# Performance work log

Hardware: AMD Instinct MI355X
Metric: run time of the kernel (lower is better)

The kernel has to match this reference:

```python
import jax, jax.numpy as jnp
import numpy as np

EPS = 1e-8
ALPHA = 0.3
PATTERN_W = 0.1


def setup_inputs() -> dict:
    key = jax.random.key(0)
    ks = jax.random.split(key, 6)
    H, W, D, Hid = 1024, 1024, 32, 64
    return {
        "grid_states": jax.random.normal(ks[0], (H, W, D), dtype=jnp.float32),
        "potentials": jax.random.uniform(ks[1], (H, W), dtype=jnp.float32),
        "W1": jax.random.normal(ks[2], (D + 1, Hid), dtype=jnp.float32) * 0.1,
        "b1": jax.random.normal(ks[3], (Hid,), dtype=jnp.float32) * 0.1,
        "W2": jax.random.normal(ks[4], (Hid, D), dtype=jnp.float32) * 0.1,
        "b2": jax.random.normal(ks[5], (D,), dtype=jnp.float32) * 0.1,
    }


def reference(grid_states, potentials, W1, b1, W2, b2):
    # self_similarity: A^3 normalized to unit length, rescaled by ||A||
    cube = grid_states * grid_states * grid_states                     # [H,W,D]
    cube_norm = jnp.linalg.norm(cube, axis=-1, keepdims=True)          # [H,W,1]
    cell_norm = jnp.linalg.norm(grid_states, axis=-1, keepdims=True)   # [H,W,1]
    self_pattern = cube / (cube_norm + EPS) * cell_norm                # [H,W,D]

    cell_with_pattern = grid_states + PATTERN_W * self_pattern         # [H,W,D]

    # transform_net on [cell_with_pattern ; potential]
    x = jnp.concatenate([cell_with_pattern, potentials[..., None]], axis=-1)  # [H,W,D+1]
    h = jax.nn.relu(jnp.einsum("hwc,cf->hwf", x, W1) + b1)             # [H,W,Hid]
    transformed = jnp.einsum("hwf,fd->hwd", h, W2) + b2                # [H,W,D]

    # new_state = transform + alpha * cell  (neighbor influence path only
    # affects role_value, which forward() discards)
    return transformed + ALPHA * grid_states
```

## Files before the change

### kernel.cpp

```cpp
#include <hip/hip_runtime.h>

#define DIM   32
#define HID   64
#define TILES 8
#define HPAD  72
#define HBUF  (16 * HPAD)

typedef __attribute__((ext_vector_type(8))) short bf16x8;
typedef __attribute__((ext_vector_type(4))) float f32x4;

__device__ __forceinline__ unsigned cvt_pk_bf16(float lo, float hi) {
    unsigned r;
    asm("v_cvt_pk_bf16_f32 %0, %1, %2" : "=v"(r) : "v"(lo), "v"(hi));
    return r;
}

union bfu { bf16x8 v; unsigned u[4]; };

__global__ __launch_bounds__(256) void behavior_mfma(
    const float* __restrict__ g_in,
    const float* __restrict__ pot,
    const float* __restrict__ W1,
    const float* __restrict__ b1,
    const float* __restrict__ W2,
    const float* __restrict__ b2,
    float* __restrict__ out)
{
    __shared__ __align__(16) short sH[4 * 2 * HBUF];

    const int tid  = threadIdx.x;
    const int lane = tid & 63;
    const int quad = lane >> 4;
    const int mrow = lane & 15;
    const int wave = tid >> 6;
    short* hb = &sH[wave * 2 * HBUF];

    bf16x8 w1f[4];
    float  w1p[4], b1v[4];
    #pragma unroll
    for (int nb = 0; nb < 4; ++nb) {
        bfu t;
        #pragma unroll
        for (int jp = 0; jp < 4; ++jp)
            t.u[jp] = cvt_pk_bf16(W1[(quad * 8 + 2 * jp)     * HID + nb * 16 + mrow],
                                  W1[(quad * 8 + 2 * jp + 1) * HID + nb * 16 + mrow]);
        w1f[nb] = t.v;
        w1p[nb] = W1[32 * HID + nb * 16 + mrow];
        b1v[nb] = b1[nb * 16 + mrow];
    }
    bf16x8 w2f[2][2];
    #pragma unroll
    for (int kc = 0; kc < 2; ++kc)
        #pragma unroll
        for (int nc = 0; nc < 2; ++nc) {
            bfu t;
            #pragma unroll
            for (int jp = 0; jp < 4; ++jp)
                t.u[jp] = cvt_pk_bf16(W2[(kc * 32 + quad * 8 + 2 * jp)     * DIM + nc * 16 + mrow],
                                      W2[(kc * 32 + quad * 8 + 2 * jp + 1) * DIM + nc * 16 + mrow]);
            w2f[kc][nc] = t.v;
        }
    float b2v[2];
    #pragma unroll
    for (int nc = 0; nc < 2; ++nc) b2v[nc] = b2[nc * 16 + mrow];

    bf16x8 idf[2];
    #pragma unroll
    for (int nc = 0; nc < 2; ++nc) {
        bfu t;
        #pragma unroll
        for (int jp = 0; jp < 4; ++jp) {
            unsigned lo = (quad * 8 + 2 * jp     == nc * 16 + mrow) ? 0x00003F80u : 0u;
            unsigned hi = (quad * 8 + 2 * jp + 1 == nc * 16 + mrow) ? 0x3F800000u : 0u;
            t.u[jp] = lo | hi;
        }
        idf[nc] = t.v;
    }

    const long cell0 = ((long)blockIdx.x * 4 + wave) * (TILES * 16);

    auto loadTile = [&](long cb, float4& a, float4& b, float4& p) {
        const float* gp = g_in + (cb + mrow) * DIM + quad * 8;
        a = ((const float4*)gp)[0];
        b = ((const float4*)gp)[1];
        p = *(const float4*)(pot + cb + quad * 4);
    };

    auto stageA = [&](const float4& a, const float4& b, const float4& p,
                      short* buf, bf16x8& gf_out) {
        float gv[8] = {a.x, a.y, a.z, a.w, b.x, b.y, b.z, b.w};
        float cube[8];
        float tp = 0.f, sp = 0.f;
        #pragma unroll
        for (int j = 0; j < 8; ++j) {
            float gc = gv[j];
            float g2 = gc * gc;
            float g3 = g2 * gc;
            tp += g2;
            sp = fmaf(g3, g3, sp);
            cube[j] = g3;
        }
        tp += __shfl_xor(tp, 16, 64); tp += __shfl_xor(tp, 32, 64);
        sp += __shfl_xor(sp, 16, 64); sp += __shfl_xor(sp, 32, 64);
        const float scale = 0.1f * __builtin_amdgcn_sqrtf(tp) *
                            __builtin_amdgcn_rcpf(__builtin_amdgcn_sqrtf(sp) + 1e-8f);

        bfu xf, gf;
        #pragma unroll
        for (int jp = 0; jp < 4; ++jp) {
            xf.u[jp] = cvt_pk_bf16(fmaf(scale, cube[2 * jp],     gv[2 * jp]),
                                   fmaf(scale, cube[2 * jp + 1], gv[2 * jp + 1]));
            gf.u[jp] = cvt_pk_bf16(0.3f * gv[2 * jp], 0.3f * gv[2 * jp + 1]);
        }
        gf_out = gf.v;

        const float pvr[4] = {p.x, p.y, p.z, p.w};
        #pragma unroll
        for (int nb = 0; nb < 4; ++nb) {
            f32x4 c1;
            #pragma unroll
            for (int r = 0; r < 4; ++r) c1[r] = fmaf(pvr[r], w1p[nb], b1v[nb]);
            c1 = __builtin_amdgcn_mfma_f32_16x16x32_bf16(xf.v, w1f[nb], c1, 0, 0, 0);
            unsigned p01 = cvt_pk_bf16(fmaxf(c1[0], 0.f), fmaxf(c1[1], 0.f));
            unsigned p23 = cvt_pk_bf16(fmaxf(c1[2], 0.f), fmaxf(c1[3], 0.f));
            short* bp = &buf[(quad * 4) * HPAD + nb * 16 + mrow];
            bp[0 * HPAD] = (short)(p01);
            bp[1 * HPAD] = (short)(p01 >> 16);
            bp[2 * HPAD] = (short)(p23);
            bp[3 * HPAD] = (short)(p23 >> 16);
        }
    };

    auto gemm2 = [&](const bf16x8& hf0, const bf16x8& hf1, const bf16x8& gfv, long cb) {
        #pragma unroll
        for (int nc = 0; nc < 2; ++nc) {
            f32x4 c2 = {b2v[nc], b2v[nc], b2v[nc], b2v[nc]};
            c2 = __builtin_amdgcn_mfma_f32_16x16x32_bf16(gfv, idf[nc],    c2, 0, 0, 0);
            c2 = __builtin_amdgcn_mfma_f32_16x16x32_bf16(hf0, w2f[0][nc], c2, 0, 0, 0);
            c2 = __builtin_amdgcn_mfma_f32_16x16x32_bf16(hf1, w2f[1][nc], c2, 0, 0, 0);
            #pragma unroll
            for (int r = 0; r < 4; ++r)
                out[(cb + quad * 4 + r) * DIM + nc * 16 + mrow] = c2[r];
        }
    };

    float4 cga, cgb, cpv, nga, ngb, npv;
    bf16x8 gfP, gfC;

    loadTile(cell0, cga, cgb, cpv);
    loadTile(cell0 + 16, nga, ngb, npv);
    stageA(cga, cgb, cpv, hb, gfP);

    #pragma unroll 2
    for (int t = 1; t < TILES; ++t) {
        short* rbuf = hb + ((t - 1) & 1) * HBUF;
        bf16x8 hf0 = *(const bf16x8*)&rbuf[mrow * HPAD +  0 + quad * 8];
        bf16x8 hf1 = *(const bf16x8*)&rbuf[mrow * HPAD + 32 + quad * 8];

        cga = nga; cgb = ngb; cpv = npv;
        if (t + 1 < TILES)
            loadTile(cell0 + (long)(t + 1) * 16, nga, ngb, npv);

        stageA(cga, cgb, cpv, hb + (t & 1) * HBUF, gfC);

        gemm2(hf0, hf1, gfP, cell0 + (long)(t - 1) * 16);
        gfP = gfC;
    }

    {
        short* rbuf = hb + ((TILES - 1) & 1) * HBUF;
        bf16x8 hf0 = *(const bf16x8*)&rbuf[mrow * HPAD +  0 + quad * 8];
        bf16x8 hf1 = *(const bf16x8*)&rbuf[mrow * HPAD + 32 + quad * 8];
        gemm2(hf0, hf1, gfP, cell0 + (long)(TILES - 1) * 16);
    }
}

extern "C" void kernel_launch(void* const* d_in, const int* in_sizes, int n_in,
                              void* d_out, int out_size, void* d_ws, size_t ws_size,
                              hipStream_t stream) {
    const float* g_in = (const float*)d_in[0];
    const float* pot  = (const float*)d_in[1];
    const float* W1   = (const float*)d_in[2];
    const float* b1   = (const float*)d_in[3];
    const float* W2   = (const float*)d_in[4];
    const float* b2   = (const float*)d_in[5];
    float* out = (float*)d_out;

    const int n_cells = in_sizes[1];
    const int cells_per_block = 4 * TILES * 16;
    const int blocks = (n_cells + cells_per_block - 1) / cells_per_block;

    behavior_mfma<<<blocks, 256, 0, stream>>>(g_in, pot, W1, b1, W2, b2, out);
}
```

Before: 247.2 us.

## Compute transposed MFMA products and pass hidden activations via permlane swaps instead of LDS

Swaps the MFMA operand order so each lane holds results for its own cell row, then rebuilds the second GEMM's hidden-activation fragments in registers with permlane32 swaps and a permuted W2 row order, removing the LDS buffer and its scalar stores and vector reloads. The row-sum reductions use a permlane swap in place of one cross-lane shuffle. Output is written as 16-byte nontemporal vector stores per lane instead of scattered scalar stores, and launch bounds request 4 blocks per CU. Removing LDS staging also drops the software pipelining across tiles, so MFMA and memory latency overlap now depends on occupancy.

Measured after the change: 256.2 us. 1.04x slower.

```diff
diff --git a/kernel.cpp b/kernel.cpp
--- a/kernel.cpp
+++ b/kernel.cpp
@@ -3,8 +3,6 @@
 #define DIM   32
 #define HID   64
 #define TILES 8
-#define HPAD  72
-#define HBUF  (16 * HPAD)
 
 typedef __attribute__((ext_vector_type(8))) short bf16x8;
 typedef __attribute__((ext_vector_type(4))) float f32x4;
@@ -15,9 +13,22 @@
     return r;
 }
 
+__device__ __forceinline__ void plswap(unsigned &a, unsigned &b) {
+    auto r = __builtin_amdgcn_permlane32_swap((int)a, (int)b, false, false);
+    a = (unsigned)r[0];
+    b = (unsigned)r[1];
+}
+
+__device__ __forceinline__ float quad_sum(float x) {
+    unsigned a = __float_as_uint(x), b = __float_as_uint(x);
+    plswap(a, b);
+    float t = __uint_as_float(a) + __uint_as_float(b);
+    return t + __shfl_xor(t, 16, 64);
+}
+
 union bfu { bf16x8 v; unsigned u[4]; };
 
-__global__ __launch_bounds__(256) void behavior_mfma(
+__global__ __launch_bounds__(256, 4) void behavior_mfma(
     const float* __restrict__ g_in,
     const float* __restrict__ pot,
     const float* __restrict__ W1,
@@ -26,17 +37,13 @@
     const float* __restrict__ b2,
     float* __restrict__ out)
 {
-    __shared__ __align__(16) short sH[4 * 2 * HBUF];
-
     const int tid  = threadIdx.x;
     const int lane = tid & 63;
     const int quad = lane >> 4;
     const int mrow = lane & 15;
     const int wave = tid >> 6;
-    short* hb = &sH[wave * 2 * HBUF];
 
     bf16x8 w1f[4];
-    float  w1p[4], b1v[4];
     #pragma unroll
     for (int nb = 0; nb < 4; ++nb) {
         bfu t;
@@ -45,8 +52,6 @@
             t.u[jp] = cvt_pk_bf16(W1[(quad * 8 + 2 * jp)     * HID + nb * 16 + mrow],
                                   W1[(quad * 8 + 2 * jp + 1) * HID + nb * 16 + mrow]);
         w1f[nb] = t.v;
-        w1p[nb] = W1[32 * HID + nb * 16 + mrow];
-        b1v[nb] = b1[nb * 16 + mrow];
     }
     bf16x8 w2f[2][2];
     #pragma unroll
@@ -55,16 +60,16 @@
         for (int nc = 0; nc < 2; ++nc) {
             bfu t;
             #pragma unroll
-            for (int jp = 0; jp < 4; ++jp)
-                t.u[jp] = cvt_pk_bf16(W2[(kc * 32 + quad * 8 + 2 * jp)     * DIM + nc * 16 + mrow],
-                                      W2[(kc * 32 + quad * 8 + 2 * jp + 1) * DIM + nc * 16 + mrow]);
+            for (int jp = 0; jp < 4; ++jp) {
+                const int j0 = 2 * jp;
+                const int r0 = kc * 32 + (quad >> 1) * 16 + (quad & 1) * 4
+                             + ((j0 >> 2) << 3) + (j0 & 3);
+                t.u[jp] = cvt_pk_bf16(W2[r0 * DIM + nc * 16 + mrow],
+                                      W2[(r0 + 1) * DIM + nc * 16 + mrow]);
+            }
             w2f[kc][nc] = t.v;
         }
-    float b2v[2];
-    #pragma unroll
-    for (int nc = 0; nc < 2; ++nc) b2v[nc] = b2[nc * 16 + mrow];
-
-    bf16x8 idf[2];
+    bf16x8 aid[2];
     #pragma unroll
     for (int nc = 0; nc < 2; ++nc) {
         bfu t;
@@ -74,20 +79,42 @@
             unsigned hi = (quad * 8 + 2 * jp + 1 == nc * 16 + mrow) ? 0x3F800000u : 0u;
             t.u[jp] = lo | hi;
         }
-        idf[nc] = t.v;
+        aid[nc] = t.v;
     }
+    float w1pq[4][4], b1q[4][4];
+    #pragma unroll
+    for (int nb = 0; nb < 4; ++nb)
+        #pragma unroll
+        for (int r = 0; r < 4; ++r) {
+            w1pq[nb][r] = W1[32 * HID + nb * 16 + quad * 4 + r];
+            b1q[nb][r]  = b1[nb * 16 + quad * 4 + r];
+        }
+    float b2q[2][4];
+    #pragma unroll
+    for (int nc = 0; nc < 2; ++nc)
+        #pragma unroll
+        for (int r = 0; r < 4; ++r)
+            b2q[nc][r] = b2[nc * 16 + quad * 4 + r];
 
     const long cell0 = ((long)blockIdx.x * 4 + wave) * (TILES * 16);
 
-    auto loadTile = [&](long cb, float4& a, float4& b, float4& p) {
+    float4 gA[2], gB[2]; float pV[2];
+    auto loadT = [&](long cb, int s) {
         const float* gp = g_in + (cb + mrow) * DIM + quad * 8;
-        a = ((const float4*)gp)[0];
-        b = ((const float4*)gp)[1];
-        p = *(const float4*)(pot + cb + quad * 4);
+        gA[s] = ((const float4*)gp)[0];
+        gB[s] = ((const float4*)gp)[1];
+        pV[s] = pot[cb + mrow];
     };
+    loadT(cell0, 0);
+    loadT(cell0 + 16, 1);
 
-    auto stageA = [&](const float4& a, const float4& b, const float4& p,
-                      short* buf, bf16x8& gf_out) {
+    #pragma unroll 2
+    for (int t = 0; t < TILES; ++t) {
+        const int s = t & 1;
+        const long cb = cell0 + (long)t * 16;
+        const float4 a = gA[s], b = gB[s];
+        const float potv = pV[s];
+
         float gv[8] = {a.x, a.y, a.z, a.w, b.x, b.y, b.z, b.w};
         float cube[8];
         float tp = 0.f, sp = 0.f;
@@ -100,8 +127,8 @@
             sp = fmaf(g3, g3, sp);
             cube[j] = g3;
         }
-        tp += __shfl_xor(tp, 16, 64); tp += __shfl_xor(tp, 32, 64);
-        sp += __shfl_xor(sp, 16, 64); sp += __shfl_xor(sp, 32, 64);
+        tp = quad_sum(tp);
+        sp = quad_sum(sp);
         const float scale = 0.1f * __builtin_amdgcn_sqrtf(tp) *
                             __builtin_amdgcn_rcpf(__builtin_amdgcn_sqrtf(sp) + 1e-8f);
 
@@ -112,66 +139,42 @@
                                    fmaf(scale, cube[2 * jp + 1], gv[2 * jp + 1]));
             gf.u[jp] = cvt_pk_bf16(0.3f * gv[2 * jp], 0.3f * gv[2 * jp + 1]);
         }
-        gf_out = gf.v;
 
-        const float pvr[4] = {p.x, p.y, p.z, p.w};
+        if (t + 2 < TILES) loadT(cb + 32, s);
+
+        unsigned P[4][2];
         #pragma unroll
         for (int nb = 0; nb < 4; ++nb) {
             f32x4 c1;
             #pragma unroll
-            for (int r = 0; r < 4; ++r) c1[r] = fmaf(pvr[r], w1p[nb], b1v[nb]);
-            c1 = __builtin_amdgcn_mfma_f32_16x16x32_bf16(xf.v, w1f[nb], c1, 0, 0, 0);
-            unsigned p01 = cvt_pk_bf16(fmaxf(c1[0], 0.f), fmaxf(c1[1], 0.f));
-            unsigned p23 = cvt_pk_bf16(fmaxf(c1[2], 0.f), fmaxf(c1[3], 0.f));
-            short* bp = &buf[(quad * 4) * HPAD + nb * 16 + mrow];
-            bp[0 * HPAD] = (short)(p01);
-            bp[1 * HPAD] = (short)(p01 >> 16);
-            bp[2 * HPAD] = (short)(p23);
-            bp[3 * HPAD] = (short)(p23 >> 16);
+            for (int r = 0; r < 4; ++r)
+                c1[r] = fmaf(potv, w1pq[nb][r], b1q[nb][r]);
+            c1 = __builtin_amdgcn_mfma_f32_16x16x32_bf16(w1f[nb], xf.v, c1, 0, 0, 0);
+            P[nb][0] = cvt_pk_bf16(fmaxf(c1[0], 0.f), fmaxf(c1[1], 0.f));
+            P[nb][1] = cvt_pk_bf16(fmaxf(c1[2], 0.f), fmaxf(c1[3], 0.f));
         }
-    };
 
-    auto gemm2 = [&](const bf16x8& hf0, const bf16x8& hf1, const bf16x8& gfv, long cb) {
+        bfu h0, h1;
+        {
+            unsigned x0 = P[0][0], y0 = P[1][0]; plswap(x0, y0);
+            unsigned x1 = P[0][1], y1 = P[1][1]; plswap(x1, y1);
+            h0.u[0] = x0; h0.u[1] = x1; h0.u[2] = y0; h0.u[3] = y1;
+        }
+        {
+            unsigned x0 = P[2][0], y0 = P[3][0]; plswap(x0, y0);
+            unsigned x1 = P[2][1], y1 = P[3][1]; plswap(x1, y1);
+            h1.u[0] = x0; h1.u[1] = x1; h1.u[2] = y0; h1.u[3] = y1;
+        }
+
         #pragma unroll
         for (int nc = 0; nc < 2; ++nc) {
-            f32x4 c2 = {b2v[nc], b2v[nc], b2v[nc], b2v[nc]};
-            c2 = __builtin_amdgcn_mfma_f32_16x16x32_bf16(gfv, idf[nc],    c2, 0, 0, 0);
-            c2 = __builtin_amdgcn_mfma_f32_16x16x32_bf16(hf0, w2f[0][nc], c2, 0, 0, 0);
-            c2 = __builtin_amdgcn_mfma_f32_16x16x32_bf16(hf1, w2f[1][nc], c2, 0, 0, 0);
-            #pragma unroll
-            for (int r = 0; r < 4; ++r)
-                out[(cb + quad * 4 + r) * DIM + nc * 16 + mrow] = c2[r];
+            f32x4 c2 = {b2q[nc][0], b2q[nc][1], b2q[nc][2], b2q[nc][3]};
+            c2 = __builtin_amdgcn_mfma_f32_16x16x32_bf16(aid[nc],    gf.v, c2, 0, 0, 0);
+            c2 = __builtin_amdgcn_mfma_f32_16x16x32_bf16(w2f[0][nc], h0.v, c2, 0, 0, 0);
+            c2 = __builtin_amdgcn_mfma_f32_16x16x32_bf16(w2f[1][nc], h1.v, c2, 0, 0, 0);
+            f32x4* op = (f32x4*)(out + (cb + mrow) * DIM + nc * 16 + quad * 4);
+            __builtin_nontemporal_store(c2, op);
         }
-    };
-
-    float4 cga, cgb, cpv, nga, ngb, npv;
-    bf16x8 gfP, gfC;
-
-    loadTile(cell0, cga, cgb, cpv);
-    loadTile(cell0 + 16, nga, ngb, npv);
-    stageA(cga, cgb, cpv, hb, gfP);
-
-    #pragma unroll 2
-    for (int t = 1; t < TILES; ++t) {
-        short* rbuf = hb + ((t - 1) & 1) * HBUF;
-        bf16x8 hf0 = *(const bf16x8*)&rbuf[mrow * HPAD +  0 + quad * 8];
-        bf16x8 hf1 = *(const bf16x8*)&rbuf[mrow * HPAD + 32 + quad * 8];
-
-        cga = nga; cgb = ngb; cpv = npv;
-        if (t + 1 < TILES)
-            loadTile(cell0 + (long)(t + 1) * 16, nga, ngb, npv);
-
-        stageA(cga, cgb, cpv, hb + (t & 1) * HBUF, gfC);
-
-        gemm2(hf0, hf1, gfP, cell0 + (long)(t - 1) * 16);
-        gfP = gfC;
-    }
-
-    {
-        short* rbuf = hb + ((TILES - 1) & 1) * HBUF;
-        bf16x8 hf0 = *(const bf16x8*)&rbuf[mrow * HPAD +  0 + quad * 8];
-        bf16x8 hf1 = *(const bf16x8*)&rbuf[mrow * HPAD + 32 + quad * 8];
-        gemm2(hf0, hf1, gfP, cell0 + (long)(TILES - 1) * 16);
     }
 }
 
```
